# Kernel optimization log

Measured on AMD Instinct MI355X. Metric: run time of the kernel, lower is better.

## Reference

```python
import jax, jax.numpy as jnp
import numpy as np
import math

B, S, D, H, F = 2, 2048, 1024, 16, 4096
HD = D // H  # head size 64
EPS = 1e-5


def layernorm(x, g, b):
    mu = jnp.mean(x, axis=-1, keepdims=True)
    var = jnp.mean((x - mu) ** 2, axis=-1, keepdims=True)
    return (x - mu) * jax.lax.rsqrt(var + EPS) * g + b


def new_gelu(x):
    c = math.sqrt(2.0 / math.pi)
    return 0.5 * x * (1.0 + jnp.tanh(c * (x + 0.044715 * x ** 3)))


def setup_inputs() -> dict:
    key = jax.random.key(0)
    ks = jax.random.split(key, 20)
    sc = 0.02
    return {
        "x": jax.random.normal(ks[0], (B, S, D), jnp.float32),
        # per-head q/k/v weights stacked: [H, HD, D] (torch Linear weight layout [out,in])
        "Wq": jax.random.normal(ks[1], (H, HD, D), jnp.float32) * sc,
        "bq": jax.random.normal(ks[2], (H, HD), jnp.float32) * sc,
        "Wk": jax.random.normal(ks[3], (H, HD, D), jnp.float32) * sc,
        "bk": jax.random.normal(ks[4], (H, HD), jnp.float32) * sc,
        "Wv": jax.random.normal(ks[5], (H, HD, D), jnp.float32) * sc,
        "bv": jax.random.normal(ks[6], (H, HD), jnp.float32) * sc,
        "Wo": jax.random.normal(ks[7], (D, D), jnp.float32) * sc,
        "bo": jax.random.normal(ks[8], (D,), jnp.float32) * sc,
        "ln1_g": 1.0 + jax.random.normal(ks[9], (D,), jnp.float32) * sc,
        "ln1_b": jax.random.normal(ks[10], (D,), jnp.float32) * sc,
        "W1": jax.random.normal(ks[11], (F, D), jnp.float32) * sc,
        "b1": jax.random.normal(ks[12], (F,), jnp.float32) * sc,
        "W2": jax.random.normal(ks[13], (D, F), jnp.float32) * sc,
        "b2": jax.random.normal(ks[14], (D,), jnp.float32) * sc,
        "ln2_g": 1.0 + jax.random.normal(ks[15], (D,), jnp.float32) * sc,
        "ln2_b": jax.random.normal(ks[16], (D,), jnp.float32) * sc,
    }


def reference(x, Wq, bq, Wk, bk, Wv, bv, Wo, bo, ln1_g, ln1_b, W1, b1, W2, b2, ln2_g, ln2_b):
    # --- pre-LN multi-head attention (dropout is identity in eval) ---
    h = layernorm(x, ln1_g, ln1_b)
    q = jnp.einsum("bsd,hed->bshe", h, Wq) + bq  # [B,S,H,HD]
    k = jnp.einsum("bsd,hed->bshe", h, Wk) + bk
    v = jnp.einsum("bsd,hed->bshe", h, Wv) + bv
    scores = jnp.einsum("bshe,bthe->bhst", q, k) / math.sqrt(HD)
    probs = jax.nn.softmax(scores, axis=-1)
    attn = jnp.einsum("bhst,bthe->bshe", probs, v).reshape(B, S, D)  # concat heads
    attn = attn @ Wo.T + bo
    x = x + attn
    # --- pre-LN MLP with NewGELU ---
    h2 = layernorm(x, ln2_g, ln2_b)
    mlp = new_gelu(h2 @ W1.T + b1) @ W2.T + b2
    return x + mlp
```

## Files before the change

### kernel.cpp

```cpp
#include <hip/hip_runtime.h>

typedef unsigned short u16;
typedef __attribute__((ext_vector_type(8))) __bf16 bf16x8;
typedef __attribute__((ext_vector_type(4))) __bf16 bf16x4;
typedef __attribute__((ext_vector_type(4))) float f32x4;
typedef __attribute__((ext_vector_type(4))) unsigned short u16x4;

#define AS1 __attribute__((address_space(1)))
#define AS3 __attribute__((address_space(3)))

__device__ __forceinline__ void async_load16(const void* g, void* l) {
  __builtin_amdgcn_global_load_lds((const AS1 void*)g, (AS3 void*)l, 16, 0, 0);
}

__device__ __forceinline__ float exp2_fast(float x) {
#if __has_builtin(__builtin_amdgcn_exp2f)
  return __builtin_amdgcn_exp2f(x);
#else
  return exp2f(x);
#endif
}
__device__ __forceinline__ float rcp_fast(float x) {
#if __has_builtin(__builtin_amdgcn_rcpf)
  return __builtin_amdgcn_rcpf(x);
#else
  return 1.0f / x;
#endif
}

__device__ __forceinline__ u16 f2bf(float f) {
  union { float f; unsigned u; } a; a.f = f;
  unsigned u = a.u;
  u += 0x7fffu + ((u >> 16) & 1u);
  return (u16)(u >> 16);
}
__device__ __forceinline__ u16 bf_bits(float f) {
  union { __bf16 b; u16 u; } c; c.b = (__bf16)f; return c.u;
}

__global__ __launch_bounds__(256)
void f2b_kernel(const float* __restrict__ s, u16* __restrict__ d, int n4) {
  int i = blockIdx.x * 256 + threadIdx.x;
  if (i >= n4) return;
  const float4 v = ((const float4*)s)[i];
  u16x4 o; o[0] = f2bf(v.x); o[1] = f2bf(v.y); o[2] = f2bf(v.z); o[3] = f2bf(v.w);
  ((u16x4*)d)[i] = o;
}

__global__ __launch_bounds__(256)
void ln_kernel(const float* __restrict__ x, const float* __restrict__ g,
               const float* __restrict__ b, u16* __restrict__ out) {
  const int row = blockIdx.x, tid = threadIdx.x;
  const float4 v = ((const float4*)(x + (size_t)row * 1024))[tid];
  float s = v.x + v.y + v.z + v.w;
  float s2 = v.x * v.x + v.y * v.y + v.z * v.z + v.w * v.w;
#pragma unroll
  for (int o = 1; o < 64; o <<= 1) { s += __shfl_xor(s, o); s2 += __shfl_xor(s2, o); }
  __shared__ float red[8];
  const int wave = tid >> 6, lane = tid & 63;
  if (lane == 0) { red[wave] = s; red[wave + 4] = s2; }
  __syncthreads();
  s = red[0] + red[1] + red[2] + red[3];
  s2 = red[4] + red[5] + red[6] + red[7];
  const float mu = s * (1.f / 1024.f);
  const float rstd = rsqrtf(s2 * (1.f / 1024.f) - mu * mu + 1e-5f);
  const float4 gg = ((const float4*)g)[tid];
  const float4 bb = ((const float4*)b)[tid];
  u16x4 o4;
  o4[0] = f2bf((v.x - mu) * rstd * gg.x + bb.x);
  o4[1] = f2bf((v.y - mu) * rstd * gg.y + bb.y);
  o4[2] = f2bf((v.z - mu) * rstd * gg.z + bb.z);
  o4[3] = f2bf((v.w - mu) * rstd * gg.w + bb.w);
  ((u16x4*)(out + (size_t)row * 1024))[tid] = o4;
}

template <int BN, class Epi>
__global__ __launch_bounds__(256)
void gemm_bt(const u16* __restrict__ A, const u16* __restrict__ Bw, int K, Epi epi) {
  constexpr int NT = BN / 32;
  constexpr int BLB = BN / 64;
  __shared__ __align__(16) u16 As[128 * 32];
  __shared__ __align__(16) u16 Bs[BN * 32];
  const int tid = threadIdx.x;
  const int wave = tid >> 6, lane = tid & 63;
  const int quad = lane >> 4, l16 = lane & 15;
  const int bm = blockIdx.x * 128, bn = blockIdx.y * BN;
  const int wm = (wave & 1) * 64, wn = (wave >> 1) * (BN / 2);

  const int srow = lane >> 2, scol = (lane & 3) * 8;
  const u16* pa0 = A + (size_t)(bm + wave * 32 + srow) * K + scol;
  const u16* pa1 = pa0 + (size_t)16 * K;
  const u16* pb0 = Bw + (size_t)(bn + wave * 16 * BLB + srow) * K + scol;
  const u16* pb1 = pb0 + (size_t)16 * K;
  u16* la0 = &As[wave * 1024];
  u16* la1 = la0 + 512;
  u16* lb0 = &Bs[wave * 512 * BLB];
  u16* lb1 = lb0 + 512;

  const f32x4 fz = {0.f, 0.f, 0.f, 0.f};
  f32x4 acc[4][NT];
#pragma unroll
  for (int i = 0; i < 4; i++)
#pragma unroll
    for (int j = 0; j < NT; j++) acc[i][j] = fz;

  for (int k0 = 0; k0 < K; k0 += 32) {
    async_load16(pa0, la0);
    async_load16(pa1, la1);
    async_load16(pb0, lb0);
    if (BLB == 2) async_load16(pb1, lb1);
    pa0 += 32; pa1 += 32; pb0 += 32; pb1 += 32;
    __syncthreads();
    bf16x8 af[4], bfr[NT];
#pragma unroll
    for (int mi = 0; mi < 4; mi++)
      af[mi] = *(const bf16x8*)&As[(wm + mi * 16 + l16) * 32 + quad * 8];
#pragma unroll
    for (int ni = 0; ni < NT; ni++)
      bfr[ni] = *(const bf16x8*)&Bs[(wn + ni * 16 + l16) * 32 + quad * 8];
#pragma unroll
    for (int mi = 0; mi < 4; mi++)
#pragma unroll
      for (int ni = 0; ni < NT; ni++)
        acc[mi][ni] = __builtin_amdgcn_mfma_f32_16x16x32_bf16(af[mi], bfr[ni], acc[mi][ni], 0, 0, 0);
    __syncthreads();
  }
#pragma unroll
  for (int mi = 0; mi < 4; mi++)
#pragma unroll
    for (int ni = 0; ni < NT; ni++)
      epi(bm + wm + mi * 16 + quad * 4, bn + wn + ni * 16 + l16, acc[mi][ni]);
}

struct EpiQKV {
  u16 *q, *k, *vt; const float *bq, *bk, *bv;
  __device__ void operator()(int m0, int n, f32x4 v) const {
    const int which = n >> 10, nn = n & 1023;
    const int hh = nn >> 6, e = nn & 63;
    const int bb = m0 >> 11, s0 = m0 & 2047;
    const size_t bh = (size_t)(bb * 16 + hh);
    if (which == 0) {
      const float bias = bq[nn];
      u16* p = &q[(bh * 2048 + s0) * 64 + e];
#pragma unroll
      for (int r = 0; r < 4; r++) p[r * 64] = bf_bits((v[r] + bias) * 0.18033688f);
    } else if (which == 1) {
      const float bias = bk[nn];
      u16* p = &k[(bh * 2048 + s0) * 64 + e];
#pragma unroll
      for (int r = 0; r < 4; r++) p[r * 64] = bf_bits(v[r] + bias);
    } else {
      const float bias = bv[nn];
      bf16x4 pk;
#pragma unroll
      for (int r = 0; r < 4; r++) pk[r] = (__bf16)(v[r] + bias);
      *(bf16x4*)&vt[(bh * 64 + e) * 2048 + s0] = pk;
    }
  }
};
struct EpiO {
  const float* x; const float* bo; float* out;
  __device__ void operator()(int m0, int n, f32x4 v) const {
    const float bias = bo[n];
#pragma unroll
    for (int r = 0; r < 4; r++) {
      const size_t i = (size_t)(m0 + r) * 1024 + n;
      out[i] = x[i] + v[r] + bias;
    }
  }
};
struct EpiGelu {
  const float* b1; u16* o;
  __device__ void operator()(int m0, int n, f32x4 v) const {
    const float bias = b1[n];
#pragma unroll
    for (int r = 0; r < 4; r++) {
      const float u = v[r] + bias;
      const float z2 = u * (2.3021183f + 0.10294515f * u * u);
      const float d = 1.0f + exp2_fast(-z2);
      o[(size_t)(m0 + r) * 4096 + n] = bf_bits(u * rcp_fast(d));
    }
  }
};
struct EpiOut {
  const float* b2; float* out;
  __device__ void operator()(int m0, int n, f32x4 v) const {
    const float bias = b2[n];
#pragma unroll
    for (int r = 0; r < 4; r++) {
      const size_t i = (size_t)(m0 + r) * 1024 + n;
      out[i] += v[r] + bias;
    }
  }
};

__global__ __launch_bounds__(256)
void attn_kernel(const u16* __restrict__ Q, const u16* __restrict__ K,
                 const u16* __restrict__ Vt, u16* __restrict__ O) {
  __shared__ __align__(16) u16 Ks[64 * 72];
  __shared__ __align__(16) u16 Vs[64 * 72];
  __shared__ __align__(16) u16 Ps[4][32 * 72];
  const int tid = threadIdx.x, wave = tid >> 6, lane = tid & 63;
  const int quad = lane >> 4, l16 = lane & 15;
  const int b = blockIdx.z, h = blockIdx.y, qt = blockIdx.x;
  const size_t bh = (size_t)(b * 16 + h);
  const u16* Qp = Q + bh * (size_t)(2048 * 64);
  const u16* Kp = K + bh * (size_t)(2048 * 64);
  const u16* Vp = Vt + bh * (size_t)(64 * 2048);
  const int q0 = qt * 128 + wave * 32;

  bf16x8 qf[2][2];
#pragma unroll
  for (int rg = 0; rg < 2; rg++) {
    const u16* qrow = &Qp[(size_t)(q0 + rg * 16 + l16) * 64 + quad * 8];
    qf[rg][0] = *(const bf16x8*)qrow;
    qf[rg][1] = *(const bf16x8*)(qrow + 32);
  }

  const int sr = tid >> 2, sc = (tid & 3) * 16;
  const int krow = 4 * (sr & 15) + (sr >> 4);
  const u16* kg = &Kp[(size_t)krow * 64 + sc];
  const u16* vg = &Vp[(size_t)sr * 2048 + sc];
  u16* kl = &Ks[sr * 72 + sc];
  u16* vl = &Vs[sr * 72 + sc];
  u16* Pw = &Ps[wave][0];

  bf16x8 ones;
#pragma unroll
  for (int i = 0; i < 8; i++) ones[i] = (__bf16)1.0f;

  const f32x4 fz = {0.f, 0.f, 0.f, 0.f};
  f32x4 acc[2][4], lsum[2];
#pragma unroll
  for (int rg = 0; rg < 2; rg++) {
    lsum[rg] = fz;
#pragma unroll
    for (int g = 0; g < 4; g++) acc[rg][g] = fz;
  }

  bf16x8 pk0 = *(const bf16x8*)kg, pk1 = *(const bf16x8*)(kg + 8);
  bf16x8 pv0 = *(const bf16x8*)vg, pv1 = *(const bf16x8*)(vg + 8);

  for (int t0 = 0; t0 < 2048; t0 += 64) {
    *(bf16x8*)kl = pk0; *(bf16x8*)(kl + 8) = pk1;
    *(bf16x8*)vl = pv0; *(bf16x8*)(vl + 8) = pv1;
    __syncthreads();
    kg += 64 * 64; vg += 64;
    pk0 = *(const bf16x8*)kg; pk1 = *(const bf16x8*)(kg + 8);
    pv0 = *(const bf16x8*)vg; pv1 = *(const bf16x8*)(vg + 8);

    f32x4 s[2][4];
#pragma unroll
    for (int g = 0; g < 4; g++) {
      const u16* kr = &Ks[(g * 16 + l16) * 72 + quad * 8];
      const bf16x8 kb0 = *(const bf16x8*)kr;
      const bf16x8 kb1 = *(const bf16x8*)(kr + 32);
#pragma unroll
      for (int rg = 0; rg < 2; rg++) {
        f32x4 z = __builtin_amdgcn_mfma_f32_16x16x32_bf16(qf[rg][0], kb0, fz, 0, 0, 0);
        s[rg][g] = __builtin_amdgcn_mfma_f32_16x16x32_bf16(qf[rg][1], kb1, z, 0, 0, 0);
      }
    }
#pragma unroll
    for (int rg = 0; rg < 2; rg++)
#pragma unroll
      for (int r = 0; r < 4; r++) {
        f32x4 pf;
#pragma unroll
        for (int g = 0; g < 4; g++) pf[g] = exp2_fast(s[rg][g][r]);
        const bf16x4 pb = __builtin_convertvector(pf, bf16x4);
        *(bf16x4*)&Pw[(rg * 16 + quad * 4 + r) * 72 + 4 * l16] = pb;
      }
    bf16x8 pa[2][2];
#pragma unroll
    for (int rg = 0; rg < 2; rg++) {
      const u16* pr = &Pw[(rg * 16 + l16) * 72 + quad * 8];
      pa[rg][0] = *(const bf16x8*)pr;
      pa[rg][1] = *(const bf16x8*)(pr + 32);
      lsum[rg] = __builtin_amdgcn_mfma_f32_16x16x32_bf16(pa[rg][0], ones, lsum[rg], 0, 0, 0);
      lsum[rg] = __builtin_amdgcn_mfma_f32_16x16x32_bf16(pa[rg][1], ones, lsum[rg], 0, 0, 0);
    }
#pragma unroll
    for (int g = 0; g < 4; g++) {
      const u16* vr = &Vs[(g * 16 + l16) * 72 + quad * 8];
      const bf16x8 vb0 = *(const bf16x8*)vr;
      const bf16x8 vb1 = *(const bf16x8*)(vr + 32);
#pragma unroll
      for (int rg = 0; rg < 2; rg++) {
        acc[rg][g] = __builtin_amdgcn_mfma_f32_16x16x32_bf16(pa[rg][0], vb0, acc[rg][g], 0, 0, 0);
        acc[rg][g] = __builtin_amdgcn_mfma_f32_16x16x32_bf16(pa[rg][1], vb1, acc[rg][g], 0, 0, 0);
      }
    }
    __syncthreads();
  }
#pragma unroll
  for (int rg = 0; rg < 2; rg++)
#pragma unroll
    for (int r = 0; r < 4; r++) {
      const float inv = rcp_fast(lsum[rg][r]);
      const int s_row = q0 + rg * 16 + quad * 4 + r;
      u16* op = (u16*)&O[((size_t)(b * 2048 + s_row)) * 1024 + h * 64 + l16];
#pragma unroll
      for (int g = 0; g < 4; g++) op[g * 16] = bf_bits(acc[rg][g][r] * inv);
    }
}

extern "C" void kernel_launch(void* const* d_in, const int* in_sizes, int n_in,
                              void* d_out, int out_size, void* d_ws, size_t ws_size,
                              hipStream_t stream) {
  const float* x   = (const float*)d_in[0];
  const float* Wq  = (const float*)d_in[1];
  const float* bq  = (const float*)d_in[2];
  const float* Wk  = (const float*)d_in[3];
  const float* bk  = (const float*)d_in[4];
  const float* Wv  = (const float*)d_in[5];
  const float* bv  = (const float*)d_in[6];
  const float* Wo  = (const float*)d_in[7];
  const float* bo  = (const float*)d_in[8];
  const float* g1  = (const float*)d_in[9];
  const float* be1 = (const float*)d_in[10];
  const float* W1  = (const float*)d_in[11];
  const float* b1  = (const float*)d_in[12];
  const float* W2  = (const float*)d_in[13];
  const float* b2  = (const float*)d_in[14];
  const float* g2  = (const float*)d_in[15];
  const float* be2 = (const float*)d_in[16];
  float* out = (float*)d_out;

  char* w = (char*)d_ws;
  u16* wqkv = (u16*)w; w += (size_t)3072 * 1024 * 2;
  u16* wob  = (u16*)w; w += (size_t)1024 * 1024 * 2;
  u16* w1b  = (u16*)w; w += (size_t)4096 * 1024 * 2;
  u16* w2b  = (u16*)w; w += (size_t)1024 * 4096 * 2;
  u16* hb   = (u16*)w; w += (size_t)4096 * 1024 * 2;
  u16* qb   = (u16*)w; w += (size_t)4096 * 1024 * 2;
  u16* kb   = (u16*)w; w += (size_t)4096 * 1024 * 2;
  u16* vtb  = (u16*)w; w += (size_t)4096 * 1024 * 2;
  u16* atb  = (u16*)w; w += (size_t)4096 * 1024 * 2;
  u16* m1b  = (u16*)w; w += (size_t)4096 * 4096 * 2;

  f2b_kernel<<<1024, 256, 0, stream>>>(Wq, wqkv, 262144);
  f2b_kernel<<<1024, 256, 0, stream>>>(Wk, wqkv + 1024 * 1024, 262144);
  f2b_kernel<<<1024, 256, 0, stream>>>(Wv, wqkv + 2 * 1024 * 1024, 262144);
  f2b_kernel<<<1024, 256, 0, stream>>>(Wo, wob, 262144);
  f2b_kernel<<<4096, 256, 0, stream>>>(W1, w1b, 1048576);
  f2b_kernel<<<4096, 256, 0, stream>>>(W2, w2b, 1048576);

  ln_kernel<<<4096, 256, 0, stream>>>(x, g1, be1, hb);
  gemm_bt<128, EpiQKV><<<dim3(32, 24), 256, 0, stream>>>(hb, wqkv, 1024,
      EpiQKV{qb, kb, vtb, bq, bk, bv});
  attn_kernel<<<dim3(16, 16, 2), 256, 0, stream>>>(qb, kb, vtb, atb);
  gemm_bt<64, EpiO><<<dim3(32, 16), 256, 0, stream>>>(atb, wob, 1024, EpiO{x, bo, out});
  ln_kernel<<<4096, 256, 0, stream>>>(out, g2, be2, hb);
  gemm_bt<128, EpiGelu><<<dim3(32, 32), 256, 0, stream>>>(hb, w1b, 1024, EpiGelu{b1, m1b});
  gemm_bt<64, EpiOut><<<dim3(32, 16), 256, 0, stream>>>(m1b, w2b, 4096, EpiOut{b2, out});
}
```

Measured before the change: 398.1 us.

## Use split-K 128x128 tiles for narrow GEMMs and fuse residual reduction into LayerNorm

The two N=1024 GEMMs (output projection and MLP down-projection) now use 128x128 tiles with a two-way split over K. Each half writes fp32 partials into reused workspace buffers. The first reduction is fused with the bias, the residual add and the second LayerNorm; a new add2 kernel sums the down-projection partials with the bias into the output. This trades the 64-wide tiles, which gave 512 blocks with less reuse, for larger tiles while keeping 512 blocks. The cost is extra fp32 partial traffic and one more kernel launch.

Result: no change. 391.9 us (-1.6%).

```diff
diff --git a/kernel.cpp b/kernel.cpp
--- a/kernel.cpp
+++ b/kernel.cpp
@@ -74,67 +74,122 @@
   ((u16x4*)(out + (size_t)row * 1024))[tid] = o4;
 }
 
-template <int BN, class Epi>
-__global__ __launch_bounds__(256)
-void gemm_bt(const u16* __restrict__ A, const u16* __restrict__ Bw, int K, Epi epi) {
-  constexpr int NT = BN / 32;
-  constexpr int BLB = BN / 64;
+__global__ __launch_bounds__(256)
+void ln_fuse(const float* __restrict__ x, const float* __restrict__ p0,
+             const float* __restrict__ p1, const float* __restrict__ bo,
+             const float* __restrict__ g, const float* __restrict__ b,
+             float* __restrict__ out, u16* __restrict__ hb) {
+  const int row = blockIdx.x, tid = threadIdx.x;
+  const size_t base = (size_t)row * 1024;
+  const float4 xv = ((const float4*)(x + base))[tid];
+  const float4 a0 = ((const float4*)(p0 + base))[tid];
+  const float4 a1 = ((const float4*)(p1 + base))[tid];
+  const float4 bv = ((const float4*)bo)[tid];
+  float4 t;
+  t.x = xv.x + a0.x + a1.x + bv.x;
+  t.y = xv.y + a0.y + a1.y + bv.y;
+  t.z = xv.z + a0.z + a1.z + bv.z;
+  t.w = xv.w + a0.w + a1.w + bv.w;
+  ((float4*)(out + base))[tid] = t;
+  float s = t.x + t.y + t.z + t.w;
+  float s2 = t.x * t.x + t.y * t.y + t.z * t.z + t.w * t.w;
+#pragma unroll
+  for (int o = 1; o < 64; o <<= 1) { s += __shfl_xor(s, o); s2 += __shfl_xor(s2, o); }
+  __shared__ float red[8];
+  const int wave = tid >> 6, lane = tid & 63;
+  if (lane == 0) { red[wave] = s; red[wave + 4] = s2; }
+  __syncthreads();
+  s = red[0] + red[1] + red[2] + red[3];
+  s2 = red[4] + red[5] + red[6] + red[7];
+  const float mu = s * (1.f / 1024.f);
+  const float rstd = rsqrtf(s2 * (1.f / 1024.f) - mu * mu + 1e-5f);
+  const float4 gg = ((const float4*)g)[tid];
+  const float4 bb = ((const float4*)b)[tid];
+  u16x4 o4;
+  o4[0] = f2bf((t.x - mu) * rstd * gg.x + bb.x);
+  o4[1] = f2bf((t.y - mu) * rstd * gg.y + bb.y);
+  o4[2] = f2bf((t.z - mu) * rstd * gg.z + bb.z);
+  o4[3] = f2bf((t.w - mu) * rstd * gg.w + bb.w);
+  ((u16x4*)(hb + base))[tid] = o4;
+}
+
+__global__ __launch_bounds__(256)
+void add2(float* __restrict__ out, const float* __restrict__ m0,
+          const float* __restrict__ m1, const float* __restrict__ b2) {
+  const int i = blockIdx.x * 256 + threadIdx.x;
+  const float4 o = ((const float4*)out)[i];
+  const float4 a = ((const float4*)m0)[i];
+  const float4 c = ((const float4*)m1)[i];
+  const float4 bv = ((const float4*)b2)[i & 255];
+  float4 r;
+  r.x = o.x + a.x + c.x + bv.x;
+  r.y = o.y + a.y + c.y + bv.y;
+  r.z = o.z + a.z + c.z + bv.z;
+  r.w = o.w + a.w + c.w + bv.w;
+  ((float4*)out)[i] = r;
+}
+
+template <class Epi>
+__global__ __launch_bounds__(256)
+void gemm_bt(const u16* __restrict__ A, const u16* __restrict__ Bw,
+             int ldk, int K, Epi epi) {
   __shared__ __align__(16) u16 As[128 * 32];
-  __shared__ __align__(16) u16 Bs[BN * 32];
+  __shared__ __align__(16) u16 Bs[128 * 32];
   const int tid = threadIdx.x;
   const int wave = tid >> 6, lane = tid & 63;
   const int quad = lane >> 4, l16 = lane & 15;
-  const int bm = blockIdx.x * 128, bn = blockIdx.y * BN;
-  const int wm = (wave & 1) * 64, wn = (wave >> 1) * (BN / 2);
+  const int bm = blockIdx.x * 128, bn = blockIdx.y * 128;
+  const int kz = blockIdx.z;
+  const int wm = (wave & 1) * 64, wn = (wave >> 1) * 64;
 
   const int srow = lane >> 2, scol = (lane & 3) * 8;
-  const u16* pa0 = A + (size_t)(bm + wave * 32 + srow) * K + scol;
-  const u16* pa1 = pa0 + (size_t)16 * K;
-  const u16* pb0 = Bw + (size_t)(bn + wave * 16 * BLB + srow) * K + scol;
-  const u16* pb1 = pb0 + (size_t)16 * K;
+  const u16* pa0 = A + (size_t)(bm + wave * 32 + srow) * ldk + (size_t)kz * K + scol;
+  const u16* pa1 = pa0 + (size_t)16 * ldk;
+  const u16* pb0 = Bw + (size_t)(bn + wave * 32 + srow) * ldk + (size_t)kz * K + scol;
+  const u16* pb1 = pb0 + (size_t)16 * ldk;
   u16* la0 = &As[wave * 1024];
   u16* la1 = la0 + 512;
-  u16* lb0 = &Bs[wave * 512 * BLB];
+  u16* lb0 = &Bs[wave * 1024];
   u16* lb1 = lb0 + 512;
 
   const f32x4 fz = {0.f, 0.f, 0.f, 0.f};
-  f32x4 acc[4][NT];
+  f32x4 acc[4][4];
 #pragma unroll
   for (int i = 0; i < 4; i++)
 #pragma unroll
-    for (int j = 0; j < NT; j++) acc[i][j] = fz;
+    for (int j = 0; j < 4; j++) acc[i][j] = fz;
 
   for (int k0 = 0; k0 < K; k0 += 32) {
     async_load16(pa0, la0);
     async_load16(pa1, la1);
     async_load16(pb0, lb0);
-    if (BLB == 2) async_load16(pb1, lb1);
+    async_load16(pb1, lb1);
     pa0 += 32; pa1 += 32; pb0 += 32; pb1 += 32;
     __syncthreads();
-    bf16x8 af[4], bfr[NT];
+    bf16x8 af[4], bfr[4];
 #pragma unroll
     for (int mi = 0; mi < 4; mi++)
       af[mi] = *(const bf16x8*)&As[(wm + mi * 16 + l16) * 32 + quad * 8];
 #pragma unroll
-    for (int ni = 0; ni < NT; ni++)
+    for (int ni = 0; ni < 4; ni++)
       bfr[ni] = *(const bf16x8*)&Bs[(wn + ni * 16 + l16) * 32 + quad * 8];
 #pragma unroll
     for (int mi = 0; mi < 4; mi++)
 #pragma unroll
-      for (int ni = 0; ni < NT; ni++)
+      for (int ni = 0; ni < 4; ni++)
         acc[mi][ni] = __builtin_amdgcn_mfma_f32_16x16x32_bf16(af[mi], bfr[ni], acc[mi][ni], 0, 0, 0);
     __syncthreads();
   }
 #pragma unroll
   for (int mi = 0; mi < 4; mi++)
 #pragma unroll
-    for (int ni = 0; ni < NT; ni++)
-      epi(bm + wm + mi * 16 + quad * 4, bn + wn + ni * 16 + l16, acc[mi][ni]);
+    for (int ni = 0; ni < 4; ni++)
+      epi(bm + wm + mi * 16 + quad * 4, bn + wn + ni * 16 + l16, kz, acc[mi][ni]);
 }
 
 struct EpiQKV {
   u16 *q, *k, *vt; const float *bq, *bk, *bv;
-  __device__ void operator()(int m0, int n, f32x4 v) const {
+  __device__ void operator()(int m0, int n, int, f32x4 v) const {
     const int which = n >> 10, nn = n & 1023;
     const int hh = nn >> 6, e = nn & 63;
     const int bb = m0 >> 11, s0 = m0 & 2047;
@@ -158,20 +213,17 @@
     }
   }
 };
-struct EpiO {
-  const float* x; const float* bo; float* out;
-  __device__ void operator()(int m0, int n, f32x4 v) const {
-    const float bias = bo[n];
-#pragma unroll
-    for (int r = 0; r < 4; r++) {
-      const size_t i = (size_t)(m0 + r) * 1024 + n;
-      out[i] = x[i] + v[r] + bias;
-    }
+struct EpiPart {
+  float *p0, *p1;
+  __device__ void operator()(int m0, int n, int kz, f32x4 v) const {
+    float* p = kz ? p1 : p0;
+#pragma unroll
+    for (int r = 0; r < 4; r++) p[(size_t)(m0 + r) * 1024 + n] = v[r];
   }
 };
 struct EpiGelu {
   const float* b1; u16* o;
-  __device__ void operator()(int m0, int n, f32x4 v) const {
+  __device__ void operator()(int m0, int n, int, f32x4 v) const {
     const float bias = b1[n];
 #pragma unroll
     for (int r = 0; r < 4; r++) {
@@ -179,17 +231,6 @@
       const float z2 = u * (2.3021183f + 0.10294515f * u * u);
       const float d = 1.0f + exp2_fast(-z2);
       o[(size_t)(m0 + r) * 4096 + n] = bf_bits(u * rcp_fast(d));
-    }
-  }
-};
-struct EpiOut {
-  const float* b2; float* out;
-  __device__ void operator()(int m0, int n, f32x4 v) const {
-    const float bias = b2[n];
-#pragma unroll
-    for (int r = 0; r < 4; r++) {
-      const size_t i = (size_t)(m0 + r) * 1024 + n;
-      out[i] += v[r] + bias;
     }
   }
 };
@@ -339,6 +380,11 @@
   u16* atb  = (u16*)w; w += (size_t)4096 * 1024 * 2;
   u16* m1b  = (u16*)w; w += (size_t)4096 * 4096 * 2;
 
+  float* p0 = (float*)m1b;
+  float* p1 = (float*)(m1b + 4096 * 2048);
+  float* m0 = (float*)qb;
+  float* m1 = (float*)vtb;
+
   f2b_kernel<<<1024, 256, 0, stream>>>(Wq, wqkv, 262144);
   f2b_kernel<<<1024, 256, 0, stream>>>(Wk, wqkv + 1024 * 1024, 262144);
   f2b_kernel<<<1024, 256, 0, stream>>>(Wv, wqkv + 2 * 1024 * 1024, 262144);
@@ -347,11 +393,15 @@
   f2b_kernel<<<4096, 256, 0, stream>>>(W2, w2b, 1048576);
 
   ln_kernel<<<4096, 256, 0, stream>>>(x, g1, be1, hb);
-  gemm_bt<128, EpiQKV><<<dim3(32, 24), 256, 0, stream>>>(hb, wqkv, 1024,
+  gemm_bt<EpiQKV><<<dim3(32, 24, 1), 256, 0, stream>>>(hb, wqkv, 1024, 1024,
       EpiQKV{qb, kb, vtb, bq, bk, bv});
   attn_kernel<<<dim3(16, 16, 2), 256, 0, stream>>>(qb, kb, vtb, atb);
-  gemm_bt<64, EpiO><<<dim3(32, 16), 256, 0, stream>>>(atb, wob, 1024, EpiO{x, bo, out});
-  ln_kernel<<<4096, 256, 0, stream>>>(out, g2, be2, hb);
-  gemm_bt<128, EpiGelu><<<dim3(32, 32), 256, 0, stream>>>(hb, w1b, 1024, EpiGelu{b1, m1b});
-  gemm_bt<64, EpiOut><<<dim3(32, 16), 256, 0, stream>>>(m1b, w2b, 4096, EpiOut{b2, out});
-}
+  gemm_bt<EpiPart><<<dim3(32, 8, 2), 256, 0, stream>>>(atb, wob, 1024, 512,
+      EpiPart{p0, p1});
+  ln_fuse<<<4096, 256, 0, stream>>>(x, p0, p1, bo, g2, be2, out, hb);
+  gemm_bt<EpiGelu><<<dim3(32, 32, 1), 256, 0, stream>>>(hb, w1b, 1024, 1024,
+      EpiGelu{b1, m1b});
+  gemm_bt<EpiPart><<<dim3(32, 8, 2), 256, 0, stream>>>(m1b, w2b, 4096, 2048,
+      EpiPart{m0, m1});
+  add2<<<4096, 256, 0, stream>>>(out, m0, m1, b2);
+}
```
